# Kernel tuning notes

Measured on AMD Instinct MI355X. Metric: run time of the kernel, lower is better.

## Reference

```python
import jax, jax.numpy as jnp
import numpy as np

B, S, D = 4, 4096, 256


def _complex_linear(x_r, x_i, w_r, w_i):
    # torch nn.Linear: y = x @ W.T ; complex mult: (Wr + i Wi)(xr + i xi)
    real = x_r @ w_r.T - x_i @ w_i.T
    imag = x_i @ w_r.T + x_r @ w_i.T
    return real, imag


def setup_inputs() -> dict:
    key = jax.random.key(0)
    ks = jax.random.split(key, 8)
    std = 1.0 / np.sqrt(D)  # ~ nn.Linear default init scale
    return {
        "query_real": jax.random.normal(ks[0], (B, S, D), jnp.float32),
        "query_imag": jax.random.normal(ks[1], (B, S, D), jnp.float32),
        "wq_real": jax.random.normal(ks[2], (D, D), jnp.float32) * std,
        "wq_imag": jax.random.normal(ks[3], (D, D), jnp.float32) * std,
        "wk_real": jax.random.normal(ks[4], (D, D), jnp.float32) * std,
        "wk_imag": jax.random.normal(ks[5], (D, D), jnp.float32) * std,
        "wv_real": jax.random.normal(ks[6], (D, D), jnp.float32) * std,
        "wv_imag": jax.random.normal(ks[7], (D, D), jnp.float32) * std,
    }


def reference(query_real, query_imag, wq_real, wq_imag, wk_real, wk_imag, wv_real, wv_imag):
    dim = query_real.shape[-1]
    scale = dim ** (-0.5)  # faithful: uses dim, not 2*dim

    q_r, q_i = _complex_linear(query_real, query_imag, wq_real, wq_imag)
    k_r, k_i = _complex_linear(query_real, query_imag, wk_real, wk_imag)
    v_r, v_i = _complex_linear(query_real, query_imag, wv_real, wv_imag)

    q_flat = jnp.concatenate([q_r, q_i], axis=-1)  # [B,S,2D]
    k_flat = jnp.concatenate([k_r, k_i], axis=-1)  # [B,S,2D]

    scores = jnp.einsum('bqd,bkd->bqk', q_flat, k_flat) * scale  # [B,S,S]
    attn = jax.nn.softmax(scores, axis=-1)

    out_r = jnp.einsum('bqk,bkd->bqd', attn, v_r)
    out_i = jnp.einsum('bqk,bkd->bqd', attn, v_i)
    return out_r, out_i, attn
```

## Files before the change

kernel.cpp:

```cpp
#include <hip/hip_runtime.h>
#include <hip/hip_fp16.h>

typedef _Float16 f16;
typedef _Float16 f16x8 __attribute__((ext_vector_type(8)));
typedef _Float16 f16x4 __attribute__((ext_vector_type(4)));
typedef float f32x4 __attribute__((ext_vector_type(4)));

#define AS1 __attribute__((address_space(1)))
#define AS3 __attribute__((address_space(3)))

__device__ __forceinline__ void g2l16(const void* g, void* l) {
  __builtin_amdgcn_global_load_lds((const AS1 void*)g, (AS3 void*)l, 16, 0, 0);
}

__device__ __forceinline__ void xcd_swz(int& bx, int& by, int& bz) {
  int gx = gridDim.x, gy = gridDim.y;
  int nwg = gx * gy * gridDim.z;
  int lin = (blockIdx.z * gy + blockIdx.y) * gx + blockIdx.x;
  int swz = (lin & 7) * (nwg >> 3) + (lin >> 3);
  bx = swz % gx;
  int t = swz / gx;
  by = t % gy;
  bz = t / gy;
}

__global__ __launch_bounds__(256) void build_x(const float* __restrict__ qr,
                                               const float* __restrict__ qi,
                                               f16* __restrict__ X) {
  long i = (long)blockIdx.x * 256 + threadIdx.x;
  long e = i * 4;
  int m = (int)(e >> 9);
  int k = (int)(e & 511);
  const float* src = (k < 256) ? (qr + (long)m * 256 + k)
                               : (qi + (long)m * 256 + (k - 256));
  float4 v = *(const float4*)src;
  f16x4 h = {(f16)v.x, (f16)v.y, (f16)v.z, (f16)v.w};
  *(f16x4*)(X + e) = h;
}

__global__ __launch_bounds__(256) void build_w(const float* __restrict__ wqr,
                                               const float* __restrict__ wqi,
                                               const float* __restrict__ wkr,
                                               const float* __restrict__ wki,
                                               const float* __restrict__ wvr,
                                               const float* __restrict__ wvi,
                                               f16* __restrict__ W) {
  long i = (long)blockIdx.x * 256 + threadIdx.x;
  long e = i * 4;
  int n = (int)(e >> 9);
  int k = (int)(e & 511);
  int sel = n >> 8;
  int row = n & 255;
  int k2 = k & 255;
  bool hi = (k >= 256);
  const float *Wr, *Wi;
  if ((sel >> 1) == 0)      { Wr = wqr; Wi = wqi; }
  else if ((sel >> 1) == 1) { Wr = wkr; Wi = wki; }
  else                      { Wr = wvr; Wi = wvi; }
  const float* src;
  float sgn = 1.0f;
  if ((sel & 1) == 0) {
    if (!hi) src = Wr + (long)row * 256 + k2;
    else   { src = Wi + (long)row * 256 + k2; sgn = -1.0f; }
  } else {
    if (!hi) src = Wi + (long)row * 256 + k2;
    else     src = Wr + (long)row * 256 + k2;
  }
  float4 v = *(const float4*)src;
  f16x4 h = {(f16)(sgn * v.x), (f16)(sgn * v.y), (f16)(sgn * v.z), (f16)(sgn * v.w)};
  *(f16x4*)(W + e) = h;
}

template <int MODE>
__global__ __launch_bounds__(512, 4) void gemm_nt(const f16* __restrict__ A, int lda, long astr,
                                                  const f16* __restrict__ B, int ldb, long bstr,
                                                  int K, float scale,
                                                  void* __restrict__ C0, long cstr,
                                                  float2* __restrict__ stats) {
  __shared__ __align__(16) f16 As[256 * 64];
  __shared__ __align__(16) f16 Bs[128 * 64];
  int bx, by, bz;
  xcd_swz(bx, by, bz);
  const f16* Ab = A + (long)bz * astr;
  const f16* Bb = B + (long)bz * bstr;
  const int tid = threadIdx.x;
  const int wave = tid >> 6, lane = tid & 63;
  const int bm = by * 256, bn = bx * 128;
  const int wm = (wave >> 1) * 64, wn = (wave & 1) * 64;
  const int lr = lane & 15, lg = lane >> 4;

  const int srow = wave * 8 + (lane >> 3);
  const int sk = ((lane & 7) ^ (lane >> 3)) * 8;

  f32x4 acc[4][4] = {};

  for (int kt = 0; kt < K; kt += 64) {
#pragma unroll
    for (int it = 0; it < 4; ++it)
      g2l16(Ab + (long)(bm + srow + it * 64) * lda + kt + sk,
            (char*)As + it * 8192 + wave * 1024);
#pragma unroll
    for (int it = 0; it < 2; ++it)
      g2l16(Bb + (long)(bn + srow + it * 64) * ldb + kt + sk,
            (char*)Bs + it * 8192 + wave * 1024);
    __syncthreads();
#pragma unroll
    for (int kk = 0; kk < 2; ++kk) {
      f16x8 af[4], bf[4];
#pragma unroll
      for (int f = 0; f < 4; ++f) {
        int sw = ((kk * 4 + lg) ^ (lr & 7)) * 8;
        af[f] = *(const f16x8*)(As + (wm + f * 16 + lr) * 64 + sw);
        bf[f] = *(const f16x8*)(Bs + (wn + f * 16 + lr) * 64 + sw);
      }
#pragma unroll
      for (int fm = 0; fm < 4; ++fm)
#pragma unroll
        for (int fn = 0; fn < 4; ++fn)
          acc[fm][fn] = __builtin_amdgcn_mfma_f32_16x16x32_f16(af[fm], bf[fn], acc[fm][fn], 0, 0, 0);
    }
    __syncthreads();
  }

#pragma unroll
  for (int fm = 0; fm < 4; ++fm) {
#pragma unroll
    for (int fn = 0; fn < 4; ++fn) {
#pragma unroll
      for (int r = 0; r < 4; ++r) {
        int row = bm + wm + fm * 16 + lg * 4 + r;
        int col = bn + wn + fn * 16 + lr;
        float v = acc[fm][fn][r];
        if (MODE == 0) {
          ((f16*)C0)[(long)row * 1536 + col] = (f16)v;
        } else {
          ((f16*)C0)[(long)bz * cstr + (long)row * 4096 + col] = (f16)(v * scale);
        }
      }
    }
  }

  if (MODE == 1) {
    const int nt = bx * 2 + (wn >> 6);
#pragma unroll
    for (int fm = 0; fm < 4; ++fm) {
#pragma unroll
      for (int r = 0; r < 4; ++r) {
        float v0 = acc[fm][0][r] * scale, v1 = acc[fm][1][r] * scale;
        float v2 = acc[fm][2][r] * scale, v3 = acc[fm][3][r] * scale;
        float mt = fmaxf(fmaxf(v0, v1), fmaxf(v2, v3));
#pragma unroll
        for (int off = 8; off >= 1; off >>= 1) mt = fmaxf(mt, __shfl_xor(mt, off));
        float lt = __expf(v0 - mt) + __expf(v1 - mt) + __expf(v2 - mt) + __expf(v3 - mt);
#pragma unroll
        for (int off = 8; off >= 1; off >>= 1) lt += __shfl_xor(lt, off);
        if (lr == 0) {
          int row = bm + wm + fm * 16 + lg * 4 + r;
          stats[(long)nt * 16384 + (long)bz * 4096 + row] = make_float2(mt, lt);
        }
      }
    }
  }
}

__global__ __launch_bounds__(256) void build_vt(const f16* __restrict__ P,
                                                f16* __restrict__ VT) {
  __shared__ f16 t[64][66];
  const int tid = threadIdx.x;
  const long b = blockIdx.z;
  const f16* src = P + (b * 4096 + (long)blockIdx.x * 64) * 1536 + 1024 + blockIdx.y * 64;
#pragma unroll
  for (int it = 0; it < 16; ++it) {
    int lin = it * 256 + tid;
    int i = lin >> 6, j = lin & 63;
    t[i][j] = src[(long)i * 1536 + j];
  }
  __syncthreads();
  f16* dst = VT + (b * 512 + (long)blockIdx.y * 64) * 4096 + blockIdx.x * 64;
#pragma unroll
  for (int it = 0; it < 16; ++it) {
    int lin = it * 256 + tid;
    int i = lin >> 6, j = lin & 63;
    dst[(long)i * 4096 + j] = t[j][i];
  }
}

__global__ __launch_bounds__(256) void merge_stats(const float2* __restrict__ stats,
                                                   float2* __restrict__ ml) {
  long row = (long)blockIdx.x * 256 + threadIdx.x;
  float m = -1e30f;
#pragma unroll 8
  for (int i = 0; i < 64; ++i) m = fmaxf(m, stats[i * 16384 + row].x);
  float l = 0.0f;
#pragma unroll 8
  for (int i = 0; i < 64; ++i) {
    float2 s = stats[i * 16384 + row];
    l += s.y * __expf(s.x - m);
  }
  ml[row] = make_float2(m, l);
}

__global__ __launch_bounds__(512, 4) void pv_fused5(const float2* __restrict__ ml,
                                                    const f16* __restrict__ S16,
                                                    const f16* __restrict__ VT,
                                                    float* __restrict__ attn,
                                                    float* __restrict__ outR,
                                                    float* __restrict__ outI) {
  __shared__ __align__(16) f16 Ps0[64 * 64];
  __shared__ __align__(16) f16 Ps1[64 * 64];
  __shared__ __align__(16) f16 Bs0[256 * 64];
  __shared__ __align__(16) f16 Bs1[256 * 64];
  int lin = blockIdx.x;
  int swz = (lin & 7) * 64 + (lin >> 3);
  int b = swz >> 7;
  int rem = swz & 127;
  int rt = rem >> 1, ch = rem & 1;
  const int bm = rt * 64;
  const int c0 = ch * 256;

  const int tid = threadIdx.x;
  const int wave = tid >> 6, lane = tid & 63;
  const int wm2 = (wave >> 2) * 32;
  const int wn2 = (wave & 3) * 64;
  const int lr = lane & 15, lg = lane >> 4;

  const int prow = tid >> 3;
  const int pc8 = tid & 7;
  const int vrow = wave * 8 + (lane >> 3);
  const int vsw = ((lane & 7) ^ ((lane >> 3) & 7)) * 8;
  float2 mlv = ml[(long)b * 4096 + bm + prow];
  const float mrow = mlv.x;
  const float invl = 1.0f / mlv.y;

  const f16* Sb = S16 + ((long)(b * 4096 + bm + prow)) * 4096 + pc8 * 8;
  float* Ab = attn + ((long)(b * 4096 + bm + prow)) * 4096 + pc8 * 8;
  const f16* Vb = VT + (long)(b * 512 + c0) * 4096;
  const int pslot = (pc8 ^ (prow & 7)) * 8;

  f32x4 acc[2][4] = {};
  f16x8 scA, scB;

#define PV_G2L(BSBUF, KT)                                                   \
  {                                                                         \
    _Pragma("unroll")                                                       \
    for (int i = 0; i < 4; ++i)                                             \
      g2l16(Vb + (long)(i * 64 + vrow) * 4096 + (KT) + vsw,                 \
            (char*)BSBUF + i * 8192 + wave * 1024);                         \
  }

#define PV_EXP(SC, PSBUF, KT, DOST)                                         \
  {                                                                         \
    float p[8];                                                             \
    _Pragma("unroll") for (int j = 0; j < 8; ++j)                           \
      p[j] = __expf((float)SC[j] - mrow) * invl;                            \
    if (DOST) {                                                             \
      float4 w0 = {p[0], p[1], p[2], p[3]};                                 \
      float4 w1 = {p[4], p[5], p[6], p[7]};                                 \
      *(float4*)(Ab + (KT)) = w0;                                           \
      *(float4*)(Ab + (KT) + 4) = w1;                                       \
    }                                                                       \
    f16x8 h = {(f16)p[0], (f16)p[1], (f16)p[2], (f16)p[3],                  \
               (f16)p[4], (f16)p[5], (f16)p[6], (f16)p[7]};                 \
    *(f16x8*)(PSBUF + prow * 64 + pslot) = h;                               \
  }

#define PV_MFMA(PSBUF, BSBUF)                                               \
  {                                                                         \
    __builtin_amdgcn_s_setprio(1);                                          \
    _Pragma("unroll")                                                       \
    for (int kk = 0; kk < 2; ++kk) {                                        \
      f16x8 af[2];                                                          \
      _Pragma("unroll")                                                     \
      for (int fm = 0; fm < 2; ++fm)                                        \
        af[fm] = *(const f16x8*)(PSBUF + (wm2 + fm * 16 + lr) * 64 +        \
                                 ((kk * 4 + lg) ^ (lr & 7)) * 8);           \
      f16x8 bf[4];                                                          \
      _Pragma("unroll")                                                     \
      for (int f = 0; f < 4; ++f)                                           \
        bf[f] = *(const f16x8*)(BSBUF + (wn2 + f * 16 + lr) * 64 +          \
                                ((kk * 4 + lg) ^ (lr & 7)) * 8);            \
      _Pragma("unroll")                                                     \
      for (int fm = 0; fm < 2; ++fm)                                        \
        _Pragma("unroll")                                                   \
        for (int f = 0; f < 4; ++f)                                         \
          acc[fm][f] = __builtin_amdgcn_mfma_f32_16x16x32_f16(              \
              af[fm], bf[f], acc[fm][f], 0, 0, 0);                          \
    }                                                                       \
    __builtin_amdgcn_s_setprio(0);                                          \
  }

#define PV_SYNC_(N)                                                         \
  asm volatile("s_waitcnt vmcnt(" #N ")" ::: "memory");                     \
  asm volatile("s_waitcnt lgkmcnt(0)" ::: "memory");                        \
  __builtin_amdgcn_s_barrier();                                             \
  __builtin_amdgcn_sched_barrier(0);
#define PV_SYNC(N) PV_SYNC_(N)

#define PV_TILE(T, BCUR, BNXT, PCUR, PNXT, SCONS, SLOAD, VMN, DOST)         \
  {                                                                         \
    PV_G2L(BNXT, ((T) + 1) * 64)                                            \
    SLOAD = *(const f16x8*)(Sb + ((T) + 2) * 64);                           \
    PV_MFMA(PCUR, BCUR)                                                     \
    PV_EXP(SCONS, PNXT, ((T) + 1) * 64, DOST)                               \
    PV_SYNC(VMN)                                                            \
  }

#define PV_RUN(VMF, VMP, VME, DOST)                                         \
  {                                                                         \
                   \
    PV_G2L(Bs0, 0)                                                          \
    scA = *(const f16x8*)(Sb + 0);                                          \
    scB = *(const f16x8*)(Sb + 64);                                         \
    PV_EXP(scA, Ps0, 0, DOST)                                               \
    PV_SYNC(VMP)                                                            \
    for (int t = 0; t < 62; t += 2) {                                       \
      PV_TILE(t, Bs0, Bs1, Ps0, Ps1, scB, scA, VMF, DOST)                   \
      PV_TILE(t + 1, Bs1, Bs0, Ps1, Ps0, scA, scB, VMF, DOST)               \
    }                                                                       \
                                        \
    {                                                                       \
      PV_G2L(Bs1, 63 * 64)                                                  \
      PV_MFMA(Ps0, Bs0)                                                     \
      PV_EXP(scB, Ps1, 63 * 64, DOST)                                       \
      PV_SYNC(VME)                                                          \
    }                                                                       \
                                                               \
    PV_MFMA(Ps1, Bs1)                                                       \
  }

  if (ch == 0) {
    PV_RUN(3, 3, 2, 1)
  } else {
    PV_RUN(1, 1, 0, 0)
  }

#undef PV_RUN
#undef PV_TILE
#undef PV_SYNC
#undef PV_SYNC_
#undef PV_MFMA
#undef PV_EXP
#undef PV_G2L

  float* outp = ch ? outI : outR;
#pragma unroll
  for (int fm = 0; fm < 2; ++fm)
#pragma unroll
    for (int f = 0; f < 4; ++f)
#pragma unroll
      for (int r = 0; r < 4; ++r) {
        int row = bm + wm2 + fm * 16 + lg * 4 + r;
        int col = wn2 + f * 16 + lr;
        outp[((long)b * 4096 + row) * 256 + col] = acc[fm][f][r];
      }
}

extern "C" void kernel_launch(void* const* d_in, const int* in_sizes, int n_in,
                              void* d_out, int out_size, void* d_ws, size_t ws_size,
                              hipStream_t stream) {
  const float* qr  = (const float*)d_in[0];
  const float* qi  = (const float*)d_in[1];
  const float* wqr = (const float*)d_in[2];
  const float* wqi = (const float*)d_in[3];
  const float* wkr = (const float*)d_in[4];
  const float* wki = (const float*)d_in[5];
  const float* wvr = (const float*)d_in[6];
  const float* wvi = (const float*)d_in[7];

  float* outR = (float*)d_out;
  float* outI = outR + (size_t)4 * 4096 * 256;
  float* attn = outI + (size_t)4 * 4096 * 256;

  const size_t offX  = 0;
  const size_t offW  = offX + (size_t)16384 * 512 * 2;
  const size_t offP  = offW + (size_t)1536 * 512 * 2;
  const size_t offVT = offP + (size_t)16384 * 1536 * 2;
  const size_t offS  = offVT + (size_t)4 * 512 * 4096 * 2;

  char* ws = (char*)d_ws;
  f16* X   = (f16*)(ws + offX);
  f16* W   = (f16*)(ws + offW);
  f16* P   = (f16*)(ws + offP);
  f16* VT  = (f16*)(ws + offVT);
  f16* S16 = (f16*)(ws + offS);
  float2* stats = (float2*)X;
  float2* ml    = (float2*)W;

  build_x<<<8192, 256, 0, stream>>>(qr, qi, X);
  build_w<<<768, 256, 0, stream>>>(wqr, wqi, wkr, wki, wvr, wvi, W);

  gemm_nt<0><<<dim3(12, 64, 1), 512, 0, stream>>>(X, 512, 0L, W, 512, 0L, 512, 1.0f,
                                                  (void*)P, 0L, nullptr);

  build_vt<<<dim3(64, 8, 4), 256, 0, stream>>>(P, VT);

  gemm_nt<1><<<dim3(32, 16, 4), 512, 0, stream>>>(P, 1536, (long)4096 * 1536,
                                                  P + 512, 1536, (long)4096 * 1536,
                                                  512, 0.0625f,
                                                  (void*)S16, (long)4096 * 4096, stats);

  merge_stats<<<64, 256, 0, stream>>>(stats, ml);

  pv_fused5<<<512, 512, 0, stream>>>(ml, S16, VT, attn, outR, outI);
}
```

Baseline: 350.6 us.

## Rewrite GEMM with double-buffered split-K LDS stages and smaller 128x128 tiles

Replaces the single-buffered 256x128 GEMM (512 threads, one sync pair per 64-wide K step) with a 128x128, 256-thread kernel. It loads each K=64 step as two 32-wide sub-stages into double-buffered LDS, using explicit vmcnt waits so the global-to-LDS loads of the next step overlap the current MFMAs. It also raises wave priority during the MFMA phase. The goal is to hide load latency in the projection and QK^T GEMMs. In exchange each tile gets less data reuse, the grid doubles, and the code relies on hand-tuned wait counts.

```diff
diff --git a/kernel.cpp b/kernel.cpp
--- a/kernel.cpp
+++ b/kernel.cpp
@@ -72,55 +72,95 @@
 }
 
 template <int MODE>
-__global__ __launch_bounds__(512, 4) void gemm_nt(const f16* __restrict__ A, int lda, long astr,
+__global__ __launch_bounds__(256, 2) void gemm_ks(const f16* __restrict__ A, int lda, long astr,
                                                   const f16* __restrict__ B, int ldb, long bstr,
                                                   int K, float scale,
                                                   void* __restrict__ C0, long cstr,
                                                   float2* __restrict__ stats) {
-  __shared__ __align__(16) f16 As[256 * 64];
-  __shared__ __align__(16) f16 Bs[128 * 64];
+  __shared__ __align__(16) f16 As[2 * 2 * 128 * 32];
+  __shared__ __align__(16) f16 Bs[2 * 2 * 128 * 32];
   int bx, by, bz;
   xcd_swz(bx, by, bz);
   const f16* Ab = A + (long)bz * astr;
   const f16* Bb = B + (long)bz * bstr;
   const int tid = threadIdx.x;
   const int wave = tid >> 6, lane = tid & 63;
-  const int bm = by * 256, bn = bx * 128;
+  const int bm = by * 128, bn = bx * 128;
   const int wm = (wave >> 1) * 64, wn = (wave & 1) * 64;
   const int lr = lane & 15, lg = lane >> 4;
 
-  const int srow = wave * 8 + (lane >> 3);
-  const int sk = ((lane & 7) ^ (lane >> 3)) * 8;
+  const int srow = wave * 32 + (lane >> 2);
+  const int ssl = ((lane & 3) ^ ((lane >> 2) & 3)) * 8;
 
   f32x4 acc[4][4] = {};
 
-  for (int kt = 0; kt < K; kt += 64) {
-#pragma unroll
-    for (int it = 0; it < 4; ++it)
-      g2l16(Ab + (long)(bm + srow + it * 64) * lda + kt + sk,
-            (char*)As + it * 8192 + wave * 1024);
-#pragma unroll
-    for (int it = 0; it < 2; ++it)
-      g2l16(Bb + (long)(bn + srow + it * 64) * ldb + kt + sk,
-            (char*)Bs + it * 8192 + wave * 1024);
-    __syncthreads();
-#pragma unroll
-    for (int kk = 0; kk < 2; ++kk) {
-      f16x8 af[4], bf[4];
-#pragma unroll
-      for (int f = 0; f < 4; ++f) {
-        int sw = ((kk * 4 + lg) ^ (lr & 7)) * 8;
-        af[f] = *(const f16x8*)(As + (wm + f * 16 + lr) * 64 + sw);
-        bf[f] = *(const f16x8*)(Bs + (wn + f * 16 + lr) * 64 + sw);
-      }
-#pragma unroll
-      for (int fm = 0; fm < 4; ++fm)
-#pragma unroll
-        for (int fn = 0; fn < 4; ++fn)
-          acc[fm][fn] = __builtin_amdgcn_mfma_f32_16x16x32_f16(af[fm], bf[fn], acc[fm][fn], 0, 0, 0);
-    }
-    __syncthreads();
-  }
+#define GK_STAGE(DN, S, KOFF)                                                 \
+  {                                                                           \
+    g2l16(Ab + (long)(bm + srow) * lda + (KOFF) + (S) * 32 + ssl,             \
+          (char*)As + ((DN) * 2 + (S)) * 8192 + wave * 2048 + lane * 16);     \
+    g2l16(Ab + (long)(bm + srow + 16) * lda + (KOFF) + (S) * 32 + ssl,        \
+          (char*)As + ((DN) * 2 + (S)) * 8192 + wave * 2048 + 1024 + lane * 16); \
+    g2l16(Bb + (long)(bn + srow) * ldb + (KOFF) + (S) * 32 + ssl,             \
+          (char*)Bs + ((DN) * 2 + (S)) * 8192 + wave * 2048 + lane * 16);     \
+    g2l16(Bb + (long)(bn + srow + 16) * ldb + (KOFF) + (S) * 32 + ssl,        \
+          (char*)Bs + ((DN) * 2 + (S)) * 8192 + wave * 2048 + 1024 + lane * 16); \
+  }
+
+#define GK_SYNC_(N)                                                           \
+  asm volatile("s_waitcnt vmcnt(" #N ")" ::: "memory");                       \
+  asm volatile("s_waitcnt lgkmcnt(0)" ::: "memory");                          \
+  __builtin_amdgcn_s_barrier();                                               \
+  __builtin_amdgcn_sched_barrier(0);
+#define GK_SYNC(N) GK_SYNC_(N)
+
+#define GK_COMPUTE(D, S)                                                      \
+  {                                                                           \
+    const f16* Ap = As + ((D) * 2 + (S)) * 4096;                              \
+    const f16* Bp = Bs + ((D) * 2 + (S)) * 4096;                              \
+    f16x8 af[4], bf[4];                                                       \
+    __builtin_amdgcn_s_setprio(1);                                            \
+    _Pragma("unroll")                                                         \
+    for (int f = 0; f < 4; ++f) {                                             \
+      int sw = (lg ^ (lr & 3)) * 8;                                           \
+      af[f] = *(const f16x8*)(Ap + (wm + f * 16 + lr) * 32 + sw);             \
+      bf[f] = *(const f16x8*)(Bp + (wn + f * 16 + lr) * 32 + sw);             \
+    }                                                                         \
+    _Pragma("unroll")                                                         \
+    for (int fm = 0; fm < 4; ++fm)                                            \
+      _Pragma("unroll")                                                       \
+      for (int fn = 0; fn < 4; ++fn)                                          \
+        acc[fm][fn] = __builtin_amdgcn_mfma_f32_16x16x32_f16(                 \
+            af[fm], bf[fn], acc[fm][fn], 0, 0, 0);                            \
+    __builtin_amdgcn_s_setprio(0);                                            \
+  }
+
+  const int nt1 = (K >> 6) - 1;
+
+  GK_STAGE(0, 0, 0)
+  GK_STAGE(0, 1, 0)
+
+  for (int t = 0; t < nt1; ++t) {
+    int d = t & 1, dn = d ^ 1;
+    int kn = (t + 1) * 64;
+    GK_STAGE(dn, 0, kn)
+    GK_SYNC(8)
+    GK_COMPUTE(d, 0)
+    GK_STAGE(dn, 1, kn)
+    GK_SYNC(8)
+    GK_COMPUTE(d, 1)
+  }
+  {
+    int dl = nt1 & 1;
+    GK_SYNC(4)
+    GK_COMPUTE(dl, 0)
+    GK_SYNC(0)
+    GK_COMPUTE(dl, 1)
+  }
+
+#undef GK_COMPUTE
+#undef GK_SYNC
+#undef GK_SYNC_
+#undef GK_STAGE
 
 #pragma unroll
   for (int fm = 0; fm < 4; ++fm) {
@@ -307,7 +347,6 @@
 
 #define PV_RUN(VMF, VMP, VME, DOST)                                         \
   {                                                                         \
-                   \
     PV_G2L(Bs0, 0)                                                          \
     scA = *(const f16x8*)(Sb + 0);                                          \
     scB = *(const f16x8*)(Sb + 64);                                         \
@@ -317,14 +356,12 @@
       PV_TILE(t, Bs0, Bs1, Ps0, Ps1, scB, scA, VMF, DOST)                   \
       PV_TILE(t + 1, Bs1, Bs0, Ps1, Ps0, scA, scB, VMF, DOST)               \
     }                                                                       \
-                                        \
     {                                                                       \
       PV_G2L(Bs1, 63 * 64)                                                  \
       PV_MFMA(Ps0, Bs0)                                                     \
       PV_EXP(scB, Ps1, 63 * 64, DOST)                                       \
       PV_SYNC(VME)                                                          \
     }                                                                       \
-                                                               \
     PV_MFMA(Ps1, Bs1)                                                       \
   }
 
@@ -389,12 +426,12 @@
   build_x<<<8192, 256, 0, stream>>>(qr, qi, X);
   build_w<<<768, 256, 0, stream>>>(wqr, wqi, wkr, wki, wvr, wvi, W);
 
-  gemm_nt<0><<<dim3(12, 64, 1), 512, 0, stream>>>(X, 512, 0L, W, 512, 0L, 512, 1.0f,
-                                                  (void*)P, 0L, nullptr);
+  gemm_ks<0><<<dim3(12, 128, 1), 256, 0, stream>>>(X, 512, 0L, W, 512, 0L, 512, 1.0f,
+                                                   (void*)P, 0L, nullptr);
 
   build_vt<<<dim3(64, 8, 4), 256, 0, stream>>>(P, VT);
 
-  gemm_nt<1><<<dim3(32, 16, 4), 512, 0, stream>>>(P, 1536, (long)4096 * 1536,
+  gemm_ks<1><<<dim3(32, 32, 4), 256, 0, stream>>>(P, 1536, (long)4096 * 1536,
                                                   P + 512, 1536, (long)4096 * 1536,
                                                   512, 0.0625f,
                                                   (void*)S16, (long)4096 * 4096, stats);
```

Result: slower. 389.7 us (+11.1%).
